# Kernel optimization log

Measured on AMD Instinct MI355X. Metric: run time of the kernel, lower is better.

The kernel has to match this reference:

```python
import jax, jax.numpy as jnp
import numpy as np

EPS = 1e-05

def setup_inputs() -> dict:
    key = jax.random.key(0)
    k1, = jax.random.split(key, 1)
    x = jax.random.normal(k1, (4, 4096, 2048), dtype=jnp.float32)
    g = jnp.ones((2048,), dtype=jnp.float32)
    return {"x": x, "g": g}

def reference(x, g):
    # RMSNorm: x / sqrt(mean(x^2, axis=-1) + eps) * g, computed in fp32
    dtype = x.dtype
    xf = x.astype(jnp.float32)
    ms = jnp.mean(xf * xf, axis=-1, keepdims=True)  # [B,S,1]
    out = xf * jax.lax.rsqrt(ms + EPS) * g
    return out.astype(dtype)
```

## Files before the change

kernel.cpp:

```cpp
#include <hip/hip_runtime.h>

#define ROW_LEN 2048
#define BLOCK   256
#define EPS     1e-5f

typedef float floatx4 __attribute__((ext_vector_type(4)));

__device__ float g_row_scale[32768];

__global__ __launch_bounds__(BLOCK) void RMSNorm_pass1_kernel(
    const float* __restrict__ x, int rows)
{
    const int wave = threadIdx.x >> 6;
    const int lane = threadIdx.x & 63;
    const int row  = blockIdx.x * (BLOCK / 64) + wave;
    if (row >= rows) return;

    const float4* __restrict__ xr =
        reinterpret_cast<const float4*>(x + (size_t)row * ROW_LEN) + lane;

    float4 v[8];
    #pragma unroll
    for (int j = 0; j < 8; ++j) v[j] = xr[j * 64];

    float s0 = 0.f, s1 = 0.f, s2 = 0.f, s3 = 0.f;
    #pragma unroll
    for (int j = 0; j < 8; ++j) {
        s0 += v[j].x * v[j].x;
        s1 += v[j].y * v[j].y;
        s2 += v[j].z * v[j].z;
        s3 += v[j].w * v[j].w;
    }
    float ss = (s0 + s1) + (s2 + s3);

    #pragma unroll
    for (int off = 32; off > 0; off >>= 1)
        ss += __shfl_xor(ss, off, 64);

    if (lane == 0)
        g_row_scale[row] = rsqrtf(ss * (1.0f / (float)ROW_LEN) + EPS);
}

__global__ __launch_bounds__(BLOCK) void RMSNorm_pass2_kernel(
    const float* __restrict__ x, const float* __restrict__ g,
    float* __restrict__ out, int n4)
{
    const floatx4* __restrict__ x4 = reinterpret_cast<const floatx4*>(x);
    const floatx4* __restrict__ g4 = reinterpret_cast<const floatx4*>(g);
    floatx4* __restrict__       o4 = reinterpret_cast<floatx4*>(out);

    const int stride = gridDim.x * BLOCK;
    for (int i = blockIdx.x * BLOCK + threadIdx.x; i < n4; i += stride) {
        const floatx4 xv = x4[i];
        const int row = i >> 9;
        const int col = i & 511;
        const float s = g_row_scale[row];
        const floatx4 gv = g4[col];
        floatx4 ov = xv * s * gv;
        __builtin_nontemporal_store(ov, &o4[i]);
    }
}

extern "C" void kernel_launch(void* const* d_in, const int* in_sizes, int n_in,
                              void* d_out, int out_size, void* d_ws, size_t ws_size,
                              hipStream_t stream) {
    const float* x = (const float*)d_in[0];
    const float* g = (const float*)d_in[1];
    float* out = (float*)d_out;

    const int rows = in_sizes[0] / ROW_LEN;
    const int n4   = rows * (ROW_LEN / 4);

    const int grid1 = (rows + (BLOCK / 64) - 1) / (BLOCK / 64);
    RMSNorm_pass1_kernel<<<grid1, BLOCK, 0, stream>>>(x, rows);

    const int grid2 = 4096;
    RMSNorm_pass2_kernel<<<grid2, BLOCK, 0, stream>>>(x, g, out, n4);
}
```

Before: 245.9 us.

## Replace per-row reduction with grid-stride atomic accumulation of row sums

```diff
diff --git a/kernel.cpp b/kernel.cpp
--- a/kernel.cpp
+++ b/kernel.cpp
@@ -6,39 +6,41 @@
 
 typedef float floatx4 __attribute__((ext_vector_type(4)));
 
-__device__ float g_row_scale[32768];
+__device__ float g_rowsum[32768];
+
+__global__ __launch_bounds__(BLOCK) void RMSNorm_zero_kernel(int rows)
+{
+    const int i = blockIdx.x * BLOCK + threadIdx.x;
+    if (i < rows) g_rowsum[i] = 0.f;
+}
 
 __global__ __launch_bounds__(BLOCK) void RMSNorm_pass1_kernel(
-    const float* __restrict__ x, int rows)
+    const float* __restrict__ x, int n4)
 {
-    const int wave = threadIdx.x >> 6;
-    const int lane = threadIdx.x & 63;
-    const int row  = blockIdx.x * (BLOCK / 64) + wave;
-    if (row >= rows) return;
+    const floatx4* __restrict__ x4 = reinterpret_cast<const floatx4*>(x);
+    const int lane   = threadIdx.x & 63;
+    const int stride = gridDim.x * BLOCK;
 
-    const float4* __restrict__ xr =
-        reinterpret_cast<const float4*>(x + (size_t)row * ROW_LEN) + lane;
+    int i = blockIdx.x * BLOCK + threadIdx.x;
+    floatx4 cur = x4[i];
 
-    float4 v[8];
-    #pragma unroll
-    for (int j = 0; j < 8; ++j) v[j] = xr[j * 64];
+    #pragma unroll 1
+    for (int it = 0; it < 8; ++it) {
+        const int inext = i + stride;
+        floatx4 nxt = cur;
+        if (it < 7) nxt = x4[inext];
 
-    float s0 = 0.f, s1 = 0.f, s2 = 0.f, s3 = 0.f;
-    #pragma unroll
-    for (int j = 0; j < 8; ++j) {
-        s0 += v[j].x * v[j].x;
-        s1 += v[j].y * v[j].y;
-        s2 += v[j].z * v[j].z;
-        s3 += v[j].w * v[j].w;
+        float s = cur.x * cur.x + cur.y * cur.y + cur.z * cur.z + cur.w * cur.w;
+        #pragma unroll
+        for (int off = 32; off > 0; off >>= 1)
+            s += __shfl_xor(s, off, 64);
+
+        if (lane == 0)
+            atomicAdd(&g_rowsum[i >> 9], s);
+
+        i = inext;
+        cur = nxt;
     }
-    float ss = (s0 + s1) + (s2 + s3);
-
-    #pragma unroll
-    for (int off = 32; off > 0; off >>= 1)
-        ss += __shfl_xor(ss, off, 64);
-
-    if (lane == 0)
-        g_row_scale[row] = rsqrtf(ss * (1.0f / (float)ROW_LEN) + EPS);
 }
 
 __global__ __launch_bounds__(BLOCK) void RMSNorm_pass2_kernel(
@@ -52,12 +54,9 @@
     const int stride = gridDim.x * BLOCK;
     for (int i = blockIdx.x * BLOCK + threadIdx.x; i < n4; i += stride) {
         const floatx4 xv = x4[i];
-        const int row = i >> 9;
-        const int col = i & 511;
-        const float s = g_row_scale[row];
-        const floatx4 gv = g4[col];
-        floatx4 ov = xv * s * gv;
-        __builtin_nontemporal_store(ov, &o4[i]);
+        const float   sc = rsqrtf(g_rowsum[i >> 9] * (1.0f / (float)ROW_LEN) + EPS);
+        const floatx4 gv = g4[i & 511];
+        __builtin_nontemporal_store(xv * sc * gv, &o4[i]);
     }
 }
 
@@ -71,9 +70,7 @@
     const int rows = in_sizes[0] / ROW_LEN;
     const int n4   = rows * (ROW_LEN / 4);
 
-    const int grid1 = (rows + (BLOCK / 64) - 1) / (BLOCK / 64);
-    RMSNorm_pass1_kernel<<<grid1, BLOCK, 0, stream>>>(x, rows);
-
-    const int grid2 = 4096;
-    RMSNorm_pass2_kernel<<<grid2, BLOCK, 0, stream>>>(x, g, out, n4);
+    RMSNorm_zero_kernel<<<(rows + BLOCK - 1) / BLOCK, BLOCK, 0, stream>>>(rows);
+    RMSNorm_pass1_kernel<<<4096, BLOCK, 0, stream>>>(x, n4);
+    RMSNorm_pass2_kernel<<<4096, BLOCK, 0, stream>>>(x, g, out, n4);
 }
```

Measured after the change: 249.4 us. Within noise of the previous version (+1.4%).
